# Optimization experiments

Hardware: AMD Instinct MI355X
Metric: run time of the kernel (lower is better)

The kernel has to match this reference:

```python
import jax, jax.numpy as jnp
from jax import lax
import numpy as np

WIN = 9  # default window [9, 9] in the original module


def _box_sum(x, win):
    """Sum over a win x win window, stride 1, pad win//2 (same as conv2d with ones kernel).
    Implemented separably (two 1D convs) - mathematically identical to the 2D ones-kernel conv.
    x: [B, 1, H, W] float32.
    """
    pad = win // 2
    kh = jnp.ones((1, 1, win, 1), x.dtype)
    kw = jnp.ones((1, 1, 1, win), x.dtype)
    dn = lax.conv_dimension_numbers(x.shape, kh.shape, ('NCHW', 'OIHW', 'NCHW'))
    y = lax.conv_general_dilated(x, kh, (1, 1), [(pad, pad), (0, 0)], dimension_numbers=dn)
    return lax.conv_general_dilated(y, kw, (1, 1), [(0, 0), (pad, pad)], dimension_numbers=dn)


def setup_inputs() -> dict:
    key = jax.random.key(0)
    k1, k2 = jax.random.split(key)
    shape = (32, 1, 512, 512)
    predict = jax.random.uniform(k1, shape, dtype=jnp.float32)
    target = jax.random.uniform(k2, shape, dtype=jnp.float32)
    return {"predict": predict, "target": target}


def reference(predict, target):
    win = WIN
    win_size = jnp.asarray(win * win, jnp.float32)

    I, J = predict, target
    I_sum = _box_sum(I, win)
    J_sum = _box_sum(J, win)
    I2_sum = _box_sum(I * I, win)
    J2_sum = _box_sum(J * J, win)
    IJ_sum = _box_sum(I * J, win)

    u_I = I_sum / win_size
    u_J = J_sum / win_size

    cross = IJ_sum - u_J * I_sum - u_I * J_sum + u_I * u_J * win_size
    I_var = I2_sum - 2.0 * u_I * I_sum + u_I * u_I * win_size
    J_var = J2_sum - 2.0 * u_J * J_sum + u_J * u_J * win_size

    cc = cross * cross / (I_var * J_var + 1e-6)
    return -jnp.mean(cc) + 1.0
```

## Files before the change

kernel.cpp:

```cpp
#include <hip/hip_runtime.h>


#define W 512
#define H 512
#define BH 4
#define NBANDS (H / BH)
#define NT 256
#define WPB 4

__device__ __forceinline__ float4 ld4(const float* p) {
    return *reinterpret_cast<const float4*>(p);
}

#define DECLBUF(P) float4 P##A0, P##A1, P##B0, P##B1; float P##m

#define PLOAD(P, DRK, SGNK) do {                                             \
    int _r  = y0 + (DRK);                                                    \
    int _rc = _r < 0 ? 0 : (_r > (H - 1) ? (H - 1) : _r);                    \
    const float* _ip = Ip + _rc * W + x0;                                    \
    const float* _jp = Jp + _rc * W + x0;                                    \
    P##A0 = ld4(_ip);     P##A1 = ld4(_ip + 4);                              \
    P##B0 = ld4(_jp);     P##B1 = ld4(_jp + 4);                              \
    P##m  = (_r == _rc) ? (SGNK) : 0.f;                                      \
} while (0)

#define PACC(P) do {                                                         \
    float _m = P##m;                                                         \
    float _a0=P##A0.x*_m, _a1=P##A0.y*_m, _a2=P##A0.z*_m, _a3=P##A0.w*_m;    \
    float _a4=P##A1.x*_m, _a5=P##A1.y*_m, _a6=P##A1.z*_m, _a7=P##A1.w*_m;    \
    float _b0=P##B0.x*_m, _b1=P##B0.y*_m, _b2=P##B0.z*_m, _b3=P##B0.w*_m;    \
    float _b4=P##B1.x*_m, _b5=P##B1.y*_m, _b6=P##B1.z*_m, _b7=P##B1.w*_m;    \
    v0[0]+=_a0; v0[1]+=_a1; v0[2]+=_a2; v0[3]+=_a3;                          \
    v0[4]+=_a4; v0[5]+=_a5; v0[6]+=_a6; v0[7]+=_a7;                          \
    v1[0]+=_b0; v1[1]+=_b1; v1[2]+=_b2; v1[3]+=_b3;                          \
    v1[4]+=_b4; v1[5]+=_b5; v1[6]+=_b6; v1[7]+=_b7;                          \
    v2[0]+=_a0*P##A0.x; v2[1]+=_a1*P##A0.y; v2[2]+=_a2*P##A0.z; v2[3]+=_a3*P##A0.w; \
    v2[4]+=_a4*P##A1.x; v2[5]+=_a5*P##A1.y; v2[6]+=_a6*P##A1.z; v2[7]+=_a7*P##A1.w; \
    v3[0]+=_b0*P##B0.x; v3[1]+=_b1*P##B0.y; v3[2]+=_b2*P##B0.z; v3[3]+=_b3*P##B0.w; \
    v3[4]+=_b4*P##B1.x; v3[5]+=_b5*P##B1.y; v3[6]+=_b6*P##B1.z; v3[7]+=_b7*P##B1.w; \
    v4[0]+=_a0*P##B0.x; v4[1]+=_a1*P##B0.y; v4[2]+=_a2*P##B0.z; v4[3]+=_a3*P##B0.w; \
    v4[4]+=_a4*P##B1.x; v4[5]+=_a5*P##B1.y; v4[6]+=_a6*P##B1.z; v4[7]+=_a7*P##B1.w; \
} while (0)

#define HLO(vv, h, l7out) do {                                               \
    float _l4 = __shfl_up(vv[4], 1), _l5 = __shfl_up(vv[5], 1);              \
    float _l6 = __shfl_up(vv[6], 1), _l7 = __shfl_up(vv[7], 1);              \
    if (lane == 0) { _l4 = 0.f; _l5 = 0.f; _l6 = 0.f; _l7 = 0.f; }           \
    float _t = (((_l4+_l5)+(_l6+_l7)) + ((vv[0]+vv[1])+(vv[2]+vv[3]))) + vv[4]; \
    h[0] = _t;                                                               \
    _t += vv[5] - _l4; h[1] = _t;                                            \
    _t += vv[6] - _l5; h[2] = _t;                                            \
    _t += vv[7] - _l6; h[3] = _t;                                            \
    l7out = _l7;                                                             \
} while (0)

#define HHI(vv, h3in, l7in, h) do {                                          \
    float _r0 = __shfl_down(vv[0], 1), _r1 = __shfl_down(vv[1], 1);          \
    float _r2 = __shfl_down(vv[2], 1), _r3 = __shfl_down(vv[3], 1);          \
    if (lane == 63) { _r0 = 0.f; _r1 = 0.f; _r2 = 0.f; _r3 = 0.f; }          \
    float _t = (h3in) + _r0 - (l7in); h[0] = _t;                             \
    _t += _r1 - vv[0]; h[1] = _t;                                            \
    _t += _r2 - vv[1]; h[2] = _t;                                            \
    _t += _r3 - vv[2]; h[3] = _t;                                            \
} while (0)

#define CC4(h0a, h1a, h2a, h3a, h4a) do {                                    \
    _Pragma("unroll")                                                        \
    for (int _c = 0; _c < 4; ++_c) {                                         \
        float _Is = h0a[_c], _Js = h1a[_c];                                  \
        float _u  = _Is * inv81;                                             \
        float _cr = h4a[_c] - _u * _Js;                                      \
        float _Iv = h2a[_c] - _u * _Is;                                      \
        float _Jv = h3a[_c] - (_Js * inv81) * _Js;                           \
        cc_acc += (_cr * _cr) * __builtin_amdgcn_rcpf(_Iv * _Jv + 1e-6f);    \
    }                                                                        \
} while (0)

#define EPI() do {                                                           \
    float h0[4], h1[4], h2[4], h3[4], h4[4];                                 \
    float s0, s1, s2, s3, s4;                                                \
    HLO(v0, h0, s0); HLO(v1, h1, s1); HLO(v2, h2, s2);                       \
    HLO(v3, h3, s3); HLO(v4, h4, s4);                                        \
    CC4(h0, h1, h2, h3, h4);                                                 \
    float e0 = h0[3], e1 = h1[3], e2 = h2[3], e3 = h3[3], e4 = h4[3];        \
    HHI(v0, e0, s0, h0); HHI(v1, e1, s1, h1); HHI(v2, e2, s2, h2);           \
    HHI(v3, e3, s3, h3); HHI(v4, e4, s4, h4);                                \
    CC4(h0, h1, h2, h3, h4);                                                 \
} while (0)

__global__ __launch_bounds__(NT, 4)
void ncc_main(const float* __restrict__ I, const float* __restrict__ J,
              float* __restrict__ partials) {
    const int lane = threadIdx.x & 63;
    const int wid  = threadIdx.x >> 6;

    const int nblk = gridDim.x;
    const int sblk = (blockIdx.x & 7) * (nblk >> 3) + (blockIdx.x >> 3);

    const int g    = sblk * WPB + wid;
    const int b    = g >> 7;
    const int band = g & (NBANDS - 1);
    const int y0   = band * BH;
    const float* Ip = I + (size_t)b * (H * W);
    const float* Jp = J + (size_t)b * (H * W);
    const int x0 = lane * 8;

    float v0[8], v1[8], v2[8], v3[8], v4[8];
    #pragma unroll
    for (int k = 0; k < 8; ++k) { v0[k]=0.f; v1[k]=0.f; v2[k]=0.f; v3[k]=0.f; v4[k]=0.f; }

    float cc_acc = 0.f;
    const float inv81 = 1.f / 81.f;

    DECLBUF(p); DECLBUF(q);

    PLOAD(p, -4, 1.f);
    PLOAD(q, -3, 1.f);
    PACC(p); PLOAD(p, -2, 1.f);
    PACC(q); PLOAD(q, -1, 1.f);
    PACC(p); PLOAD(p,  0, 1.f);
    PACC(q); PLOAD(q,  1, 1.f);
    PACC(p); PLOAD(p,  2, 1.f);
    PACC(q); PLOAD(q,  3, 1.f);
    PACC(p); PLOAD(p,  4, 1.f);
    PACC(q); PLOAD(q, -4, -1.f);
    PACC(p); PLOAD(p,  5, 1.f);
    EPI();
    PACC(q); PLOAD(q, -3, -1.f);
    PACC(p); PLOAD(p,  6, 1.f);
    EPI();
    PACC(q); PLOAD(q, -2, -1.f);
    PACC(p); PLOAD(p,  7, 1.f);
    EPI();
    PACC(q);
    PACC(p);
    EPI();

    #pragma unroll
    for (int off = 32; off > 0; off >>= 1)
        cc_acc += __shfl_down(cc_acc, off, 64);
    __shared__ float wsum[WPB];
    if (lane == 0) wsum[wid] = cc_acc;
    __syncthreads();
    if (threadIdx.x == 0)
        partials[blockIdx.x] = (wsum[0] + wsum[1]) + (wsum[2] + wsum[3]);
}

__global__ __launch_bounds__(256)
void ncc_finish(const float* __restrict__ partials, float* __restrict__ out,
                int n, float inv_total) {
    float v = 0.f;
    for (int i = threadIdx.x; i < n; i += blockDim.x) v += partials[i];
    #pragma unroll
    for (int off = 32; off > 0; off >>= 1)
        v += __shfl_down(v, off, 64);
    __shared__ float wsum[4];
    if ((threadIdx.x & 63) == 0) wsum[threadIdx.x >> 6] = v;
    __syncthreads();
    if (threadIdx.x == 0) {
        float t = (wsum[0] + wsum[1]) + (wsum[2] + wsum[3]);
        out[0] = 1.0f - t * inv_total;
    }
}

extern "C" void kernel_launch(void* const* d_in, const int* in_sizes, int n_in,
                              void* d_out, int out_size, void* d_ws, size_t ws_size,
                              hipStream_t stream) {
    const float* I = (const float*)d_in[0];
    const float* J = (const float*)d_in[1];
    float* out = (float*)d_out;
    float* partials = (float*)d_ws;

    const int n = in_sizes[0];
    const int B = n / (H * W);
    const int nblocks = B * NBANDS / WPB;

    ncc_main<<<nblocks, NT, 0, stream>>>(I, J, partials);
    ncc_finish<<<1, 256, 0, stream>>>(partials, out, nblocks, 1.0f / (float)n);
}
```

Measured before the change: 116.8 us.

## Use taller 16-row bands per wave with a 10-row sliding register buffer

Each wave now handles a 16-row band instead of 4, keeping ten rows in registers and updating the vertical window by adding the incoming row and subtracting the outgoing one. This cuts the redundant halo reads (8 extra rows per 4 output rows before, 8 per 16 now). Blocks shrink to a single wave, which removes the shared-memory reduction and the block barrier. The cost is much higher register pressure from ten row buffers, fewer waves in flight (1024 instead of 4096), and a longer serial chain of work per wave.

```diff
diff --git a/kernel.cpp b/kernel.cpp
--- a/kernel.cpp
+++ b/kernel.cpp
@@ -3,10 +3,9 @@
 
 #define W 512
 #define H 512
-#define BH 4
+#define BH 16
 #define NBANDS (H / BH)
-#define NT 256
-#define WPB 4
+#define NT 64
 
 __device__ __forceinline__ float4 ld4(const float* p) {
     return *reinterpret_cast<const float4*>(p);
@@ -14,33 +13,37 @@
 
 #define DECLBUF(P) float4 P##A0, P##A1, P##B0, P##B1; float P##m
 
-#define PLOAD(P, DRK, SGNK) do {                                             \
-    int _r  = y0 + (DRK);                                                    \
+#define LOADR(P, DR) do {                                                    \
+    int _r  = y0 + (DR);                                                     \
     int _rc = _r < 0 ? 0 : (_r > (H - 1) ? (H - 1) : _r);                    \
     const float* _ip = Ip + _rc * W + x0;                                    \
     const float* _jp = Jp + _rc * W + x0;                                    \
-    P##A0 = ld4(_ip);     P##A1 = ld4(_ip + 4);                              \
-    P##B0 = ld4(_jp);     P##B1 = ld4(_jp + 4);                              \
-    P##m  = (_r == _rc) ? (SGNK) : 0.f;                                      \
+    P##A0 = ld4(_ip);  P##A1 = ld4(_ip + 4);                                 \
+    P##B0 = ld4(_jp);  P##B1 = ld4(_jp + 4);                                 \
+    P##m  = (_r == _rc) ? 1.f : 0.f;                                         \
 } while (0)
 
-#define PACC(P) do {                                                         \
-    float _m = P##m;                                                         \
-    float _a0=P##A0.x*_m, _a1=P##A0.y*_m, _a2=P##A0.z*_m, _a3=P##A0.w*_m;    \
-    float _a4=P##A1.x*_m, _a5=P##A1.y*_m, _a6=P##A1.z*_m, _a7=P##A1.w*_m;    \
-    float _b0=P##B0.x*_m, _b1=P##B0.y*_m, _b2=P##B0.z*_m, _b3=P##B0.w*_m;    \
-    float _b4=P##B1.x*_m, _b5=P##B1.y*_m, _b6=P##B1.z*_m, _b7=P##B1.w*_m;    \
-    v0[0]+=_a0; v0[1]+=_a1; v0[2]+=_a2; v0[3]+=_a3;                          \
-    v0[4]+=_a4; v0[5]+=_a5; v0[6]+=_a6; v0[7]+=_a7;                          \
-    v1[0]+=_b0; v1[1]+=_b1; v1[2]+=_b2; v1[3]+=_b3;                          \
-    v1[4]+=_b4; v1[5]+=_b5; v1[6]+=_b6; v1[7]+=_b7;                          \
-    v2[0]+=_a0*P##A0.x; v2[1]+=_a1*P##A0.y; v2[2]+=_a2*P##A0.z; v2[3]+=_a3*P##A0.w; \
-    v2[4]+=_a4*P##A1.x; v2[5]+=_a5*P##A1.y; v2[6]+=_a6*P##A1.z; v2[7]+=_a7*P##A1.w; \
-    v3[0]+=_b0*P##B0.x; v3[1]+=_b1*P##B0.y; v3[2]+=_b2*P##B0.z; v3[3]+=_b3*P##B0.w; \
-    v3[4]+=_b4*P##B1.x; v3[5]+=_b5*P##B1.y; v3[6]+=_b6*P##B1.z; v3[7]+=_b7*P##B1.w; \
-    v4[0]+=_a0*P##B0.x; v4[1]+=_a1*P##B0.y; v4[2]+=_a2*P##B0.z; v4[3]+=_a3*P##B0.w; \
-    v4[4]+=_a4*P##B1.x; v4[5]+=_a5*P##B1.y; v4[6]+=_a6*P##B1.z; v4[7]+=_a7*P##B1.w; \
-} while (0)
+#define PBODY(P, OP)                                                         \
+    do {                                                                     \
+        float _m = P##m;                                                     \
+        float _a0=P##A0.x*_m, _a1=P##A0.y*_m, _a2=P##A0.z*_m, _a3=P##A0.w*_m;\
+        float _a4=P##A1.x*_m, _a5=P##A1.y*_m, _a6=P##A1.z*_m, _a7=P##A1.w*_m;\
+        float _b0=P##B0.x*_m, _b1=P##B0.y*_m, _b2=P##B0.z*_m, _b3=P##B0.w*_m;\
+        float _b4=P##B1.x*_m, _b5=P##B1.y*_m, _b6=P##B1.z*_m, _b7=P##B1.w*_m;\
+        v0[0] OP _a0; v0[1] OP _a1; v0[2] OP _a2; v0[3] OP _a3;              \
+        v0[4] OP _a4; v0[5] OP _a5; v0[6] OP _a6; v0[7] OP _a7;              \
+        v1[0] OP _b0; v1[1] OP _b1; v1[2] OP _b2; v1[3] OP _b3;              \
+        v1[4] OP _b4; v1[5] OP _b5; v1[6] OP _b6; v1[7] OP _b7;              \
+        v2[0] OP _a0*P##A0.x; v2[1] OP _a1*P##A0.y; v2[2] OP _a2*P##A0.z; v2[3] OP _a3*P##A0.w; \
+        v2[4] OP _a4*P##A1.x; v2[5] OP _a5*P##A1.y; v2[6] OP _a6*P##A1.z; v2[7] OP _a7*P##A1.w; \
+        v3[0] OP _b0*P##B0.x; v3[1] OP _b1*P##B0.y; v3[2] OP _b2*P##B0.z; v3[3] OP _b3*P##B0.w; \
+        v3[4] OP _b4*P##B1.x; v3[5] OP _b5*P##B1.y; v3[6] OP _b6*P##B1.z; v3[7] OP _b7*P##B1.w; \
+        v4[0] OP _a0*P##B0.x; v4[1] OP _a1*P##B0.y; v4[2] OP _a2*P##B0.z; v4[3] OP _a3*P##B0.w; \
+        v4[4] OP _a4*P##B1.x; v4[5] OP _a5*P##B1.y; v4[6] OP _a6*P##B1.z; v4[7] OP _a7*P##B1.w; \
+    } while (0)
+
+#define PADD(P) PBODY(P, +=)
+#define PSUB(P) PBODY(P, -=)
 
 #define HLO(vv, h, l7out) do {                                               \
     float _l4 = __shfl_up(vv[4], 1), _l5 = __shfl_up(vv[5], 1);              \
@@ -88,17 +91,18 @@
     CC4(h0, h1, h2, h3, h4);                                                 \
 } while (0)
 
-__global__ __launch_bounds__(NT, 4)
+#define STEPL(AB, SB, DR) do { PADD(AB); EPI(); PSUB(SB); LOADR(SB, DR); } while (0)
+#define STEPN(AB, SB)     do { PADD(AB); EPI(); PSUB(SB); } while (0)
+
+__global__ __launch_bounds__(NT)
 void ncc_main(const float* __restrict__ I, const float* __restrict__ J,
               float* __restrict__ partials) {
     const int lane = threadIdx.x & 63;
-    const int wid  = threadIdx.x >> 6;
 
     const int nblk = gridDim.x;
-    const int sblk = (blockIdx.x & 7) * (nblk >> 3) + (blockIdx.x >> 3);
+    const int g = (blockIdx.x & 7) * (nblk >> 3) + (blockIdx.x >> 3);
 
-    const int g    = sblk * WPB + wid;
-    const int b    = g >> 7;
+    const int b    = g >> 5;
     const int band = g & (NBANDS - 1);
     const int y0   = band * BH;
     const float* Ip = I + (size_t)b * (H * W);
@@ -112,38 +116,37 @@
     float cc_acc = 0.f;
     const float inv81 = 1.f / 81.f;
 
-    DECLBUF(p); DECLBUF(q);
+    DECLBUF(B0); DECLBUF(B1); DECLBUF(B2); DECLBUF(B3); DECLBUF(B4);
+    DECLBUF(B5); DECLBUF(B6); DECLBUF(B7); DECLBUF(B8); DECLBUF(B9);
 
-    PLOAD(p, -4, 1.f);
-    PLOAD(q, -3, 1.f);
-    PACC(p); PLOAD(p, -2, 1.f);
-    PACC(q); PLOAD(q, -1, 1.f);
-    PACC(p); PLOAD(p,  0, 1.f);
-    PACC(q); PLOAD(q,  1, 1.f);
-    PACC(p); PLOAD(p,  2, 1.f);
-    PACC(q); PLOAD(q,  3, 1.f);
-    PACC(p); PLOAD(p,  4, 1.f);
-    PACC(q); PLOAD(q, -4, -1.f);
-    PACC(p); PLOAD(p,  5, 1.f);
-    EPI();
-    PACC(q); PLOAD(q, -3, -1.f);
-    PACC(p); PLOAD(p,  6, 1.f);
-    EPI();
-    PACC(q); PLOAD(q, -2, -1.f);
-    PACC(p); PLOAD(p,  7, 1.f);
-    EPI();
-    PACC(q);
-    PACC(p);
-    EPI();
+    LOADR(B0, -4); LOADR(B1, -3); LOADR(B2, -2); LOADR(B3, -1);
+    LOADR(B4,  0); LOADR(B5,  1); LOADR(B6,  2); LOADR(B7,  3);
+    LOADR(B8,  4); LOADR(B9,  5);
+
+    PADD(B0); PADD(B1); PADD(B2); PADD(B3);
+    PADD(B4); PADD(B5); PADD(B6); PADD(B7);
+
+    STEPL(B8, B0,  6);
+    STEPL(B9, B1,  7);
+    STEPL(B0, B2,  8);
+    STEPL(B1, B3,  9);
+    STEPL(B2, B4, 10);
+    STEPL(B3, B5, 11);
+    STEPL(B4, B6, 12);
+    STEPL(B5, B7, 13);
+    STEPL(B6, B8, 14);
+    STEPL(B7, B9, 15);
+    STEPL(B8, B0, 16);
+    STEPL(B9, B1, 17);
+    STEPL(B0, B2, 18);
+    STEPL(B1, B3, 19);
+    STEPN(B2, B4);
+    STEPN(B3, B5);
 
     #pragma unroll
     for (int off = 32; off > 0; off >>= 1)
         cc_acc += __shfl_down(cc_acc, off, 64);
-    __shared__ float wsum[WPB];
-    if (lane == 0) wsum[wid] = cc_acc;
-    __syncthreads();
-    if (threadIdx.x == 0)
-        partials[blockIdx.x] = (wsum[0] + wsum[1]) + (wsum[2] + wsum[3]);
+    if (lane == 0) partials[blockIdx.x] = cc_acc;
 }
 
 __global__ __launch_bounds__(256)
@@ -173,7 +176,7 @@
 
     const int n = in_sizes[0];
     const int B = n / (H * W);
-    const int nblocks = B * NBANDS / WPB;
+    const int nblocks = B * NBANDS;
 
     ncc_main<<<nblocks, NT, 0, stream>>>(I, J, partials);
     ncc_finish<<<1, 256, 0, stream>>>(partials, out, nblocks, 1.0f / (float)n);
```

After: 105.8 us. 1.1x faster.
